# Kernel optimization log

Measured on AMD Instinct MI355X. Metric: run time of the kernel, lower is better.

## Reference

```python
import jax, jax.numpy as jnp
import numpy as np

B, D, Q, U = 4096, 512, 16384, 256  # batch, feat dim, CQ size, unique pids per batch
OIM_SCALAR = 30.0
IGNORE = -1


def _normalize(x):
    # F.normalize(dim=-1): divide by L2 norm clamped to eps
    n = jnp.maximum(jnp.linalg.norm(x, axis=-1, keepdims=True), 1e-12)
    return x / n


def setup_inputs() -> dict:
    key = jax.random.key(0)
    k1, k2, k3 = jax.random.split(key, 3)
    inputs = jax.random.normal(k1, (B, D), dtype=jnp.float32)
    # exactly U unique pids, each repeated B//U times, shuffled
    labels = jax.random.permutation(k2, jnp.arange(B, dtype=jnp.int32) % U)
    emb_cq = jax.random.normal(k3, (Q, D), dtype=jnp.float32)
    emb_cq = _normalize(emb_cq)  # queue stores normalized embeddings
    # unique queue labels; slice overlaps batch pids -> exercises the c==1 branch
    label_cq = jnp.arange(Q, dtype=jnp.int32) + 1000
    label_cq = label_cq.at[5000:5000 + U].set(jnp.arange(U, dtype=jnp.int32))
    age_cq = jnp.ones((Q,), dtype=jnp.int32)
    return {"inputs": inputs, "labels": labels, "emb_cq": emb_cq,
            "label_cq": label_cq, "age_cq": age_cq, "header_cq": 0}


def reference(inputs, labels, emb_cq, label_cq, age_cq, header_cq):
    # ---- per-pid masked mean (torch.unique loop, vectorized) ----
    uniq = jnp.unique(labels, size=U)                      # sorted unique pids [U]
    m_u = (uniq[:, None] == labels[None, :]).astype(inputs.dtype)  # [U,B]
    uniq_emb = (m_u @ inputs) / m_u.sum(axis=1, keepdims=True)     # [U,D]

    inputs_n = _normalize(inputs)
    uniq_emb_n = jax.lax.stop_gradient(_normalize(uniq_emb))  # queue write is under no_grad

    # ---- circular queue update (sequential, data-dependent) ----
    age_cq = age_cq + (label_cq != IGNORE).astype(age_cq.dtype)

    def step(carry, xy):
        emb, lab, age, h = carry
        x, y = xy
        m = lab == y
        c = m.any()
        i = jnp.argmax(m)          # existing slot for pid y (if any)
        emb = emb.at[h].set(x)
        lab = lab.at[h].set(y)
        age = age.at[h].set(1)
        inval = c & (i != h)       # invalidate stale slot
        lab = lab.at[i].set(jnp.where(inval, IGNORE, lab[i]))
        age = age.at[i].set(jnp.where(inval, 0, age[i]))
        return (emb, lab, age, (h + 1) % Q), None

    h0 = jnp.asarray(header_cq, dtype=jnp.int32)
    (emb_cq, label_cq, age_cq, _), _ = jax.lax.scan(
        step, (emb_cq, label_cq, age_cq, h0), (uniq_emb_n, uniq))
    emb_cq = jax.lax.stop_gradient(emb_cq)  # buffer: no grad through the queue

    # ---- cosine-sim cross-entropy over valid queue entries ----
    good = label_cq != IGNORE                               # [Q]
    # each batch pid matches exactly one good queue slot
    xe = jnp.argmax((labels[:, None] == label_cq[None, :]) & good[None, :], axis=1)
    logits = OIM_SCALAR * (inputs_n @ emb_cq.T)             # [B,Q]
    logits = jnp.where(good[None, :], logits, -jnp.inf)     # mask == compacting emb_cq[good]
    logp = jax.nn.log_softmax(logits, axis=1)
    loss = -jnp.mean(logp[jnp.arange(B), xe])               # sum(xe_i)/B
    return loss
```

## Files before the change

kernel.cpp:

```cpp
#include <hip/hip_runtime.h>
#include <hip/hip_bf16.h>

#define Bn 4096
#define Dn 512
#define Qn 16384
#define Un 256
#define OIM 30.0f


typedef int i32x4 __attribute__((ext_vector_type(4)));

__device__ __forceinline__ void async_copy16(const int4* g, int4* l) {
    __builtin_amdgcn_global_load_lds((const __attribute__((address_space(1))) void*)g,
                                     (__attribute__((address_space(3))) void*)l, 16, 0, 0);
}

__device__ __forceinline__ int clamp8(float v, float qs) {
    int q = __float2int_rn(v * qs);
    return max(-127, min(127, q));
}

__global__ void prep_kernel(const float* __restrict__ inputs, const int* __restrict__ labels,
                            const float* __restrict__ emb_cq, const int* __restrict__ label_cq,
                            const int* __restrict__ header,
                            char* __restrict__ inA8, char* __restrict__ embQ8,
                            float* __restrict__ invA, float* __restrict__ invB,
                            float* __restrict__ goodf, float* __restrict__ rowsum,
                            float* __restrict__ out) {
    __shared__ float wred[4];
    __shared__ float wmax[4];
    __shared__ int lidx[64];
    __shared__ int lcnt;
    int blk = blockIdx.x;
    int tid = threadIdx.x;
    float2 o;
    char* dst;
    float* invdst;
    int drow;
    if (blk == 0 && tid == 0) out[0] = 0.f;
    if (blk < Bn) {
        if (tid == 0) rowsum[blk] = 0.f;
        float2 v = ((const float2*)(inputs + (size_t)blk * Dn))[tid];
        float ss = v.x * v.x + v.y * v.y;
        for (int d = 1; d < 64; d <<= 1) ss += __shfl_xor(ss, d, 64);
        if ((tid & 63) == 0) wred[tid >> 6] = ss;
        __syncthreads();
        float sc = 1.0f / fmaxf(sqrtf(wred[0] + wred[1] + wred[2] + wred[3]), 1e-12f);
        o.x = v.x * sc; o.y = v.y * sc;
        dst = inA8; invdst = invA; drow = blk;
    } else {
        int j = blk - Bn;
        int h0 = header[0];
        int t = j - h0; if (t < 0) t += Qn;
        if (t < Un) {
            if (tid == 0) lcnt = 0;
            __syncthreads();
            for (int b = tid; b < Bn; b += 256)
                if (labels[b] == t) { int s = atomicAdd(&lcnt, 1); if (s < 64) lidx[s] = b; }
            __syncthreads();
            int c = lcnt; if (c > 64) c = 64;
            float2 acc = {0.f, 0.f};
            for (int s = 0; s < c; ++s) {
                float2 x = ((const float2*)(inputs + (size_t)lidx[s] * Dn))[tid];
                acc.x += x.x; acc.y += x.y;
            }
            float inv = 1.0f / (float)(c > 0 ? c : 1);
            acc.x *= inv; acc.y *= inv;
            float ss = acc.x * acc.x + acc.y * acc.y;
            for (int d = 1; d < 64; d <<= 1) ss += __shfl_xor(ss, d, 64);
            if ((tid & 63) == 0) wred[tid >> 6] = ss;
            __syncthreads();
            float sc = 1.0f / fmaxf(sqrtf(wred[0] + wred[1] + wred[2] + wred[3]), 1e-12f);
            o.x = acc.x * sc; o.y = acc.y * sc;
        } else {
            o = ((const float2*)(emb_cq + (size_t)j * Dn))[tid];
        }
        if (tid == 0) {
            int vl = label_cq[j];
            int fin = (vl >= 0 && vl < Un) ? -1 : vl;
            if (t < Un) fin = t;
            goodf[j] = (fin != -1) ? 1.0f : 0.0f;
        }
        dst = embQ8; invdst = invB; drow = j;
    }
    float am = fmaxf(fabsf(o.x), fabsf(o.y));
    for (int d = 1; d < 64; d <<= 1) am = fmaxf(am, __shfl_xor(am, d, 64));
    if ((tid & 63) == 0) wmax[tid >> 6] = am;
    __syncthreads();
    float m = fmaxf(fmaxf(fmaxf(wmax[0], wmax[1]), fmaxf(wmax[2], wmax[3])), 1e-12f);
    float qs = 127.0f / m;
    char2 pc;
    pc.x = (char)clamp8(o.x, qs);
    pc.y = (char)clamp8(o.y, qs);
    *(char2*)(dst + (size_t)drow * Dn + tid * 2) = pc;
    if (tid == 0) invdst[drow] = m / 127.0f;
}

__global__ __launch_bounds__(256, 4) void gemm_kernel(
    const char* __restrict__ inA8,
    const char* __restrict__ embQ8,
    const float* __restrict__ invA,
    const float* __restrict__ invB,
    const float* __restrict__ goodf,
    const int* __restrict__ labels,
    const int* __restrict__ header,
    float* __restrict__ rowsum,
    float* __restrict__ target)
{
    const float LOG2E = 1.4426950408889634f;
    const float LN2   = 0.6931471805599453f;
    __shared__ char As[2 * 128 * 64];
    __shared__ char Bs[2 * 128 * 64];
    __shared__ float rsl[128];
    __shared__ int tgtc[128];
    __shared__ float sAl[128], sBl[128];
    int tid = threadIdx.x;
    int lane = tid & 63, w = tid >> 6;
    int wm = w >> 1, wn = w & 1;
    int m0 = blockIdx.y * 128, n0 = blockIdx.x * 128;
    if (tid < 128) {
        rsl[tid] = 0.f;
        int tc = header[0] + labels[m0 + tid];
        if (tc >= Qn) tc -= Qn;
        tgtc[tid] = tc;
        sAl[tid] = invA[m0 + tid];
        sBl[tid] = invB[n0 + tid];
    }
    i32x4 acc[4][4] = {};
    const int4* Ag = (const int4*)(inA8 + (size_t)m0 * Dn);
    const int4* Bg = (const int4*)(embQ8 + (size_t)n0 * Dn);
    int4* As4 = (int4*)As;
    int4* Bs4 = (int4*)Bs;
    int goff[2];
    #pragma unroll
    for (int t = 0; t < 2; ++t) {
        int g = t * 256 + tid;
        int r = g >> 2, sc = g & 3;
        int c = (sc - (r >> 1)) & 3;
        goff[t] = r * 32 + c;
    }
    int q = lane >> 4;
    int offA[4], offB[4];
    #pragma unroll
    for (int i = 0; i < 4; ++i) {
        int ar = wm * 64 + i * 16 + (lane & 15);
        offA[i] = ar * 64 + (((q + (ar >> 1)) & 3) << 4);
        int br = wn * 64 + i * 16 + (lane & 15);
        offB[i] = br * 64 + (((q + (br >> 1)) & 3) << 4);
    }
    #pragma unroll
    for (int t = 0; t < 2; ++t) {
        int g = t * 256 + tid;
        async_copy16(&Ag[goff[t]], &As4[g]);
        async_copy16(&Bg[goff[t]], &Bs4[g]);
    }
    for (int kk = 0; kk < Dn / 64; ++kk) {
        int cur = kk & 1;
        __syncthreads();
        if (kk < 7) {
            int nb = (cur ^ 1) * 512;
            #pragma unroll
            for (int t = 0; t < 2; ++t) {
                int g = t * 256 + tid;
                async_copy16(&Ag[goff[t] + (kk + 1) * 4], &As4[nb + g]);
                async_copy16(&Bg[goff[t] + (kk + 1) * 4], &Bs4[nb + g]);
            }
        }
        const char* Ab = As + cur * 8192;
        const char* Bb = Bs + cur * 8192;
        i32x4 af[4], bfr[4];
        #pragma unroll
        for (int i = 0; i < 4; ++i)
            af[i] = *(const i32x4*)(Ab + offA[i]);
        #pragma unroll
        for (int j = 0; j < 4; ++j)
            bfr[j] = *(const i32x4*)(Bb + offB[j]);
        #pragma unroll
        for (int i = 0; i < 4; ++i)
            #pragma unroll
            for (int j = 0; j < 4; ++j)
                acc[i][j] = __builtin_amdgcn_mfma_i32_16x16x64_i8(af[i], bfr[j], acc[i][j], 0, 0, 0);
    }
    int colb = n0 + wn * 64 + (lane & 15);
    float gd[4], sB4[4];
    #pragma unroll
    for (int j = 0; j < 4; ++j) {
        gd[j]  = goodf[colb + j * 16];
        sB4[j] = sBl[wn * 64 + (lane & 15) + j * 16];
    }
    #pragma unroll
    for (int i = 0; i < 4; ++i) {
        #pragma unroll
        for (int r = 0; r < 4; ++r) {
            int rowl = wm * 64 + i * 16 + q * 4 + r;
            float fA = (OIM * LOG2E) * sAl[rowl];
            int tc = tgtc[rowl];
            float s = 0.f;
            #pragma unroll
            for (int j = 0; j < 4; ++j) {
                float v2 = fA * sB4[j] * (float)acc[i][j][r];
                s += gd[j] * __builtin_amdgcn_exp2f(v2);
                if (tc == colb + j * 16) target[m0 + rowl] = v2 * LN2;
            }
            #pragma unroll
            for (int d = 1; d < 16; d <<= 1) s += __shfl_xor(s, d, 64);
            if ((lane & 15) == 0)
                atomicAdd(&rsl[rowl], s);
        }
    }
    __syncthreads();
    if (tid < 128) atomicAdd(&rowsum[m0 + tid], rsl[tid]);
}

__global__ void loss_kernel(const float* __restrict__ rowsum, const float* __restrict__ target,
                            float* __restrict__ out) {
    __shared__ float red[4];
    int tid = threadIdx.x;
    int b = blockIdx.x * 256 + tid;
    float s = logf(rowsum[b]) - target[b];
    #pragma unroll
    for (int d = 1; d < 64; d <<= 1) s += __shfl_xor(s, d, 64);
    if ((tid & 63) == 0) red[tid >> 6] = s;
    __syncthreads();
    if (tid == 0)
        atomicAdd(out, (red[0] + red[1] + red[2] + red[3]) * (1.0f / (float)Bn));
}

extern "C" void kernel_launch(void* const* d_in, const int* in_sizes, int n_in,
                              void* d_out, int out_size, void* d_ws, size_t ws_size,
                              hipStream_t stream) {
    const float* inputs   = (const float*)d_in[0];
    const int*   labels   = (const int*)d_in[1];
    const float* emb_cq   = (const float*)d_in[2];
    const int*   label_cq = (const int*)d_in[3];
    const int*   header   = (const int*)d_in[5];

    char* ws = (char*)d_ws;
    size_t off = 0;
    auto alloc = [&](size_t bytes) { char* p = ws + off; off += (bytes + 255) & ~(size_t)255; return p; };
    char*  inA8   = (char*)alloc((size_t)Bn * Dn);
    char*  embQ8  = (char*)alloc((size_t)Qn * Dn);
    float* invA   = (float*)alloc(Bn * 4);
    float* invB   = (float*)alloc(Qn * 4);
    float* goodf  = (float*)alloc(Qn * 4);
    float* rowsum = (float*)alloc(Bn * 4);
    float* target = (float*)alloc(Bn * 4);

    hipLaunchKernelGGL(prep_kernel, dim3(Bn + Qn), dim3(256), 0, stream,
                       inputs, labels, emb_cq, label_cq, header,
                       inA8, embQ8, invA, invB, goodf, rowsum, (float*)d_out);
    hipLaunchKernelGGL(gemm_kernel, dim3(Qn / 128, Bn / 128), dim3(256), 0, stream,
                       inA8, embQ8, invA, invB, goodf, labels, header, rowsum, target);
    hipLaunchKernelGGL(loss_kernel, dim3(Bn / 256), dim3(256), 0, stream,
                       rowsum, target, (float*)d_out);
}
```

Before: 161.2 us.

## Pre-tile A int8 matrix in MFMA fragment layout and load directly to registers

The prep kernel now writes the normalized int8 batch matrix in a 16-row by 16-byte tiled layout that matches the MFMA A-fragment order. The GEMM kernel then loads A fragments straight from global memory into registers, double-buffered across k-steps, instead of staging A through LDS. This removes A's LDS traffic and cuts shared memory use, which may allow higher occupancy. In exchange it puts direct global-load latency on the critical path and relies on the register double buffer and cache reuse to hide it.

New measurement: 157.7 us. -2.2%, faster.

```diff
diff --git a/kernel.cpp b/kernel.cpp
--- a/kernel.cpp
+++ b/kernel.cpp
@@ -34,8 +34,7 @@
     int blk = blockIdx.x;
     int tid = threadIdx.x;
     float2 o;
-    char* dst;
-    float* invdst;
+    bool isA;
     int drow;
     if (blk == 0 && tid == 0) out[0] = 0.f;
     if (blk < Bn) {
@@ -47,7 +46,7 @@
         __syncthreads();
         float sc = 1.0f / fmaxf(sqrtf(wred[0] + wred[1] + wred[2] + wred[3]), 1e-12f);
         o.x = v.x * sc; o.y = v.y * sc;
-        dst = inA8; invdst = invA; drow = blk;
+        isA = true; drow = blk;
     } else {
         int j = blk - Bn;
         int h0 = header[0];
@@ -81,7 +80,7 @@
             if (t < Un) fin = t;
             goodf[j] = (fin != -1) ? 1.0f : 0.0f;
         }
-        dst = embQ8; invdst = invB; drow = j;
+        isA = false; drow = blk - Bn;
     }
     float am = fmaxf(fabsf(o.x), fabsf(o.y));
     for (int d = 1; d < 64; d <<= 1) am = fmaxf(am, __shfl_xor(am, d, 64));
@@ -92,8 +91,16 @@
     char2 pc;
     pc.x = (char)clamp8(o.x, qs);
     pc.y = (char)clamp8(o.y, qs);
-    *(char2*)(dst + (size_t)drow * Dn + tid * 2) = pc;
-    if (tid == 0) invdst[drow] = m / 127.0f;
+    if (isA) {
+        int kb = tid * 2;
+        size_t addr = (size_t)(drow >> 4) * 8192 + (size_t)(kb >> 4) * 256
+                    + (drow & 15) * 16 + (kb & 15);
+        *(char2*)(inA8 + addr) = pc;
+        if (tid == 0) invA[drow] = m / 127.0f;
+    } else {
+        *(char2*)(embQ8 + (size_t)drow * Dn + tid * 2) = pc;
+        if (tid == 0) invB[drow] = m / 127.0f;
+    }
 }
 
 __global__ __launch_bounds__(256, 4) void gemm_kernel(
@@ -109,7 +116,6 @@
 {
     const float LOG2E = 1.4426950408889634f;
     const float LN2   = 0.6931471805599453f;
-    __shared__ char As[2 * 128 * 64];
     __shared__ char Bs[2 * 128 * 64];
     __shared__ float rsl[128];
     __shared__ int tgtc[128];
@@ -127,9 +133,7 @@
         sBl[tid] = invB[n0 + tid];
     }
     i32x4 acc[4][4] = {};
-    const int4* Ag = (const int4*)(inA8 + (size_t)m0 * Dn);
     const int4* Bg = (const int4*)(embQ8 + (size_t)n0 * Dn);
-    int4* As4 = (int4*)As;
     int4* Bs4 = (int4*)Bs;
     int goff[2];
     #pragma unroll
@@ -140,20 +144,24 @@
         goff[t] = r * 32 + c;
     }
     int q = lane >> 4;
-    int offA[4], offB[4];
-    #pragma unroll
-    for (int i = 0; i < 4; ++i) {
-        int ar = wm * 64 + i * 16 + (lane & 15);
-        offA[i] = ar * 64 + (((q + (ar >> 1)) & 3) << 4);
-        int br = wn * 64 + i * 16 + (lane & 15);
-        offB[i] = br * 64 + (((q + (br >> 1)) & 3) << 4);
-    }
+    int offB[4];
+    #pragma unroll
+    for (int j = 0; j < 4; ++j) {
+        int br = wn * 64 + j * 16 + (lane & 15);
+        offB[j] = br * 64 + (((q + (br >> 1)) & 3) << 4);
+    }
+    const char* Ap[4];
+    #pragma unroll
+    for (int i = 0; i < 4; ++i)
+        Ap[i] = inA8 + (size_t)((m0 >> 4) + wm * 4 + i) * 8192 + lane * 16;
     #pragma unroll
     for (int t = 0; t < 2; ++t) {
         int g = t * 256 + tid;
-        async_copy16(&Ag[goff[t]], &As4[g]);
         async_copy16(&Bg[goff[t]], &Bs4[g]);
     }
+    i32x4 a0[4], a1[4];
+    #pragma unroll
+    for (int i = 0; i < 4; ++i) a0[i] = *(const i32x4*)(Ap[i]);
     for (int kk = 0; kk < Dn / 64; ++kk) {
         int cur = kk & 1;
         __syncthreads();
@@ -162,16 +170,19 @@
             #pragma unroll
             for (int t = 0; t < 2; ++t) {
                 int g = t * 256 + tid;
-                async_copy16(&Ag[goff[t] + (kk + 1) * 4], &As4[nb + g]);
                 async_copy16(&Bg[goff[t] + (kk + 1) * 4], &Bs4[nb + g]);
             }
-        }
-        const char* Ab = As + cur * 8192;
+            int off = (kk + 1) * 1024;
+            if (cur) {
+                #pragma unroll
+                for (int i = 0; i < 4; ++i) a0[i] = *(const i32x4*)(Ap[i] + off);
+            } else {
+                #pragma unroll
+                for (int i = 0; i < 4; ++i) a1[i] = *(const i32x4*)(Ap[i] + off);
+            }
+        }
         const char* Bb = Bs + cur * 8192;
-        i32x4 af[4], bfr[4];
-        #pragma unroll
-        for (int i = 0; i < 4; ++i)
-            af[i] = *(const i32x4*)(Ab + offA[i]);
+        i32x4 bfr[4];
         #pragma unroll
         for (int j = 0; j < 4; ++j)
             bfr[j] = *(const i32x4*)(Bb + offB[j]);
@@ -179,7 +190,9 @@
         for (int i = 0; i < 4; ++i)
             #pragma unroll
             for (int j = 0; j < 4; ++j)
-                acc[i][j] = __builtin_amdgcn_mfma_i32_16x16x64_i8(af[i], bfr[j], acc[i][j], 0, 0, 0);
+                acc[i][j] = cur
+                    ? __builtin_amdgcn_mfma_i32_16x16x64_i8(a1[i], bfr[j], acc[i][j], 0, 0, 0)
+                    : __builtin_amdgcn_mfma_i32_16x16x64_i8(a0[i], bfr[j], acc[i][j], 0, 0, 0);
     }
     int colb = n0 + wn * 64 + (lane & 15);
     float gd[4], sB4[4];
```
